# Performance work log

Measured on AMD Instinct MI355X. Metric: run time of the kernel, lower is better.

## Reference

```python
import jax, jax.numpy as jnp
import numpy as np
import math

SIZE = 64
SCALE = math.sqrt(SIZE)
EPS = 1e-12  # torch F.normalize default eps

def l2_normalize(x, axis):
    n = jnp.linalg.norm(x, ord=2, axis=axis, keepdims=True)
    return x / jnp.maximum(n, EPS)

def setup_inputs() -> dict:
    key = jax.random.key(0)
    k1, k2, k3 = jax.random.split(key, 3)
    n, l, s, d, v = 8, 2048, 2048, SIZE, SIZE
    return {
        "query": jax.random.normal(k1, (n, l, d), dtype=jnp.float32),
        "key": jax.random.normal(k2, (n, s, d), dtype=jnp.float32),
        "value": jax.random.normal(k3, (n, s, v), dtype=jnp.float32),
        "mask": jnp.ones((n, l, s), dtype=bool),
    }

def reference(query, key, value, mask):
    # rank-3 query path with normalize=True (cosine attention)
    q = l2_normalize(query, 2)
    k = l2_normalize(key, 2)
    score = jnp.einsum('nlk,nsk->nls', q, k) / SCALE
    score = jnp.where(mask, score, -jnp.inf)
    score = jax.nn.softmax(score, axis=2)  # [n, l, s]
    # equivalent to (score.unsqueeze(3) * value.unsqueeze(1)).sum(2)
    output_value = jnp.einsum('nls,nsv->nlv', score, value)
    return (output_value, score)
```

## Files before the change

kernel.cpp:

```cpp
#include <hip/hip_runtime.h>
#include <hip/hip_bf16.h>
#include <math.h>


typedef __bf16 bf16x8 __attribute__((ext_vector_type(8)));
typedef __bf16 bf16x4 __attribute__((ext_vector_type(4)));
typedef float f32x4 __attribute__((ext_vector_type(4)));

#define NB 8
#define LL 2048
#define SS 2048
#define DD 64
#define MWORDS 64

__global__ __launch_bounds__(512) void prep_mask(const int* __restrict__ mask,
                                                 unsigned* __restrict__ Mb) {
  __shared__ unsigned char nib[512];
  const size_t row = blockIdx.x;
  const int t = threadIdx.x;
  const int4 m = *(const int4*)(mask + row * SS + (size_t)t * 4);
  nib[t] = (unsigned char)((m.x ? 1 : 0) | (m.y ? 2 : 0) | (m.z ? 4 : 0) | (m.w ? 8 : 0));
  __syncthreads();
  if (t < MWORDS) {
    unsigned wd = 0;
#pragma unroll
    for (int i = 0; i < 8; ++i) wd |= (unsigned)nib[t * 8 + i] << (4 * i);
    Mb[row * MWORDS + t] = wd;
  }
}

__global__ __launch_bounds__(256) void prep_norm(const float* __restrict__ q,
                                                 const float* __restrict__ k,
                                                 __bf16* __restrict__ Qb,
                                                 __bf16* __restrict__ Kb) {
  int w = threadIdx.x >> 6, lane = threadIdx.x & 63;
  int r = blockIdx.x * 4 + w;
  const float* src;
  __bf16* dst;
  float extra;
  if (r < NB * LL) {
    src = q + (size_t)r * DD;
    dst = Qb + (size_t)r * DD;
    extra = 0.125f;
  } else {
    int rk = r - NB * LL;
    src = k + (size_t)rk * DD;
    dst = Kb + (size_t)rk * DD;
    extra = 1.0f;
  }
  float x = src[lane];
  float ss = x * x;
  ss += __shfl_xor(ss, 1);
  ss += __shfl_xor(ss, 2);
  ss += __shfl_xor(ss, 4);
  ss += __shfl_xor(ss, 8);
  ss += __shfl_xor(ss, 16);
  ss += __shfl_xor(ss, 32);
  float nrm = sqrtf(ss);
  float sc = extra / fmaxf(nrm, 1e-12f);
  dst[lane] = (__bf16)(x * sc);
}

__global__ __launch_bounds__(256) void prep_vt(const float* __restrict__ v,
                                               __bf16* __restrict__ Vt) {
  __shared__ __bf16 tile[64][72];
  int n = blockIdx.y;
  int s0 = blockIdx.x * 64;
  int t = threadIdx.x;
#pragma unroll
  for (int it = 0; it < 4; ++it) {
    int idx = t + it * 256;
    int s = idx >> 4, c = idx & 15;
    float4 f = *(const float4*)(v + ((size_t)(n * SS + s0 + s)) * DD + c * 4);
    tile[s][c * 4 + 0] = (__bf16)f.x;
    tile[s][c * 4 + 1] = (__bf16)f.y;
    tile[s][c * 4 + 2] = (__bf16)f.z;
    tile[s][c * 4 + 3] = (__bf16)f.w;
  }
  __syncthreads();
#pragma unroll
  for (int it = 0; it < 4; ++it) {
    int idx = t + it * 256;
    int vv = idx >> 4, c = idx & 15;
    bf16x4 o;
    o[0] = tile[c * 4 + 0][vv];
    o[1] = tile[c * 4 + 1][vv];
    o[2] = tile[c * 4 + 2][vv];
    o[3] = tile[c * 4 + 3][vv];
    *(bf16x4*)(Vt + ((size_t)(n * DD + vv)) * SS + s0 + c * 4) = o;
  }
}

__global__ __launch_bounds__(512, 4) void attn_main(const __bf16* __restrict__ Qb,
                                                    const __bf16* __restrict__ Kb,
                                                    const __bf16* __restrict__ Vt,
                                                    const unsigned* __restrict__ Mb,
                                                    float* __restrict__ out_val,
                                                    float* __restrict__ out_score) {
  __shared__ __bf16 e_lds[2][16][136];
  __shared__ float rs_lds[8][16];
  __shared__ float acc_red[4][16][17];

  const int n = blockIdx.y;
  const int l0 = blockIdx.x * 16;
  const int t = threadIdx.x;
  const int w = t >> 6;
  const int lane = t & 63;
  const int m16 = lane & 15;
  const int quad = lane >> 4;
  const int vg = w & 3;
  const int sh = (w >> 2) * 64;

  const __bf16* qrow = Qb + ((size_t)(n * LL + l0 + m16)) * DD;
  bf16x8 aq0 = *(const bf16x8*)(qrow + quad * 8);
  bf16x8 aq1 = *(const bf16x8*)(qrow + 32 + quad * 8);

  const __bf16* kbase = Kb + (size_t)n * SS * DD;
  const __bf16* vrow = Vt + ((size_t)(n * DD + vg * 16 + m16)) * SS + sh;
  const size_t mrow = ((size_t)(n * LL + l0 + m16)) * SS + w * 16 + quad * 4;
  const int off16 = w * 16 + quad * 4;
  const unsigned* mbits = Mb + ((size_t)(n * LL + l0 + m16)) * MWORDS + (off16 >> 5);
  const int bitoff = off16 & 31;

  f32x4 acc_o = {0.f, 0.f, 0.f, 0.f};
  float rsum = 0.f;
  bf16x4 stash[16];
  unsigned bw0 = mbits[0];
  unsigned bw1 = mbits[4];
  unsigned bw2 = mbits[8];
  unsigned bw3 = mbits[12];

#pragma unroll
  for (int c = 0; c < 16; ++c) {
    const int sc = c * 128;
    const int scol = sc + w * 16 + m16;
    const __bf16* krow = kbase + (size_t)scol * DD;
    bf16x8 kb0 = *(const bf16x8*)(krow + quad * 8);
    bf16x8 kb1 = *(const bf16x8*)(krow + 32 + quad * 8);
    bf16x8 bv0 = *(const bf16x8*)(vrow + sc + quad * 8);
    bf16x8 bv1 = *(const bf16x8*)(vrow + sc + 32 + quad * 8);
    f32x4 acc = {0.f, 0.f, 0.f, 0.f};
    acc = __builtin_amdgcn_mfma_f32_16x16x32_bf16(kb0, aq0, acc, 0, 0, 0);
    acc = __builtin_amdgcn_mfma_f32_16x16x32_bf16(kb1, aq1, acc, 0, 0, 0);
    unsigned bits;
    switch (c & 3) {
      case 0: bits = bw0; if (c + 4 < 16) bw0 = mbits[(c + 4) * 4]; break;
      case 1: bits = bw1; if (c + 4 < 16) bw1 = mbits[(c + 4) * 4]; break;
      case 2: bits = bw2; if (c + 4 < 16) bw2 = mbits[(c + 4) * 4]; break;
      default: bits = bw3; if (c + 4 < 16) bw3 = mbits[(c + 4) * 4]; break;
    }
    const unsigned b4 = (bits >> bitoff) & 0xFu;
    float e0 = (b4 & 1u) ? __expf(acc[0]) : 0.f;
    float e1 = (b4 & 2u) ? __expf(acc[1]) : 0.f;
    float e2 = (b4 & 4u) ? __expf(acc[2]) : 0.f;
    float e3 = (b4 & 8u) ? __expf(acc[3]) : 0.f;
    rsum += (e0 + e1) + (e2 + e3);
    bf16x4 sv;
    sv[0] = (__bf16)e0;
    sv[1] = (__bf16)e1;
    sv[2] = (__bf16)e2;
    sv[3] = (__bf16)e3;
    stash[c] = sv;
    *(bf16x4*)(&e_lds[c & 1][m16][w * 16 + quad * 4]) = sv;
    __syncthreads();
    bf16x8 ae0 = *(const bf16x8*)(&e_lds[c & 1][m16][sh + quad * 8]);
    bf16x8 ae1 = *(const bf16x8*)(&e_lds[c & 1][m16][sh + 32 + quad * 8]);
    acc_o = __builtin_amdgcn_mfma_f32_16x16x32_bf16(ae0, bv0, acc_o, 0, 0, 0);
    acc_o = __builtin_amdgcn_mfma_f32_16x16x32_bf16(ae1, bv1, acc_o, 0, 0, 0);
  }

  rsum += __shfl_xor(rsum, 16);
  rsum += __shfl_xor(rsum, 32);
  if (quad == 0) rs_lds[w][m16] = rsum;
  if (w >= 4) {
#pragma unroll
    for (int r = 0; r < 4; ++r) acc_red[vg][quad * 4 + r][m16] = acc_o[r];
  }
  __syncthreads();

  float tot = 0.f;
#pragma unroll
  for (int ww = 0; ww < 8; ++ww) tot += rs_lds[ww][m16];
  const float inv_s = 1.0f / tot;

  if (w < 4) {
#pragma unroll
    for (int r = 0; r < 4; ++r) {
      const int row = quad * 4 + r;
      float tr = 0.f;
#pragma unroll
      for (int ww = 0; ww < 8; ++ww) tr += rs_lds[ww][row];
      const float o = (acc_o[r] + acc_red[vg][row][m16]) / tr;
      out_val[((size_t)(n * LL + l0 + row)) * DD + vg * 16 + m16] = o;
    }
  }

  float* orow = out_score + mrow;
#pragma unroll
  for (int c = 0; c < 16; ++c) {
    float4 o;
    o.x = (float)stash[c][0] * inv_s;
    o.y = (float)stash[c][1] * inv_s;
    o.z = (float)stash[c][2] * inv_s;
    o.w = (float)stash[c][3] * inv_s;
    *(float4*)(orow + (size_t)c * 128) = o;
  }
}

extern "C" void kernel_launch(void* const* d_in, const int* in_sizes, int n_in,
                              void* d_out, int out_size, void* d_ws, size_t ws_size,
                              hipStream_t stream) {
  const float* q = (const float*)d_in[0];
  const float* k = (const float*)d_in[1];
  const float* v = (const float*)d_in[2];
  const int* mask = (const int*)d_in[3];

  float* out_val = (float*)d_out;
  float* out_score = out_val + (size_t)NB * LL * DD;

  __bf16* Qb = (__bf16*)d_ws;
  __bf16* Kb = Qb + (size_t)NB * LL * DD;
  __bf16* Vt = Kb + (size_t)NB * SS * DD;
  unsigned* Mb = (unsigned*)(Vt + (size_t)NB * DD * SS);

  prep_mask<<<dim3(NB * LL), dim3(512), 0, stream>>>(mask, Mb);
  prep_norm<<<dim3((NB * LL * 2) / 4), dim3(256), 0, stream>>>(q, k, Qb, Kb);
  prep_vt<<<dim3(SS / 64, NB), dim3(256), 0, stream>>>(v, Vt);
  attn_main<<<dim3(LL / 16, NB), dim3(512), 0, stream>>>(Qb, Kb, Vt, Mb, out_val, out_score);
}
```

Baseline: 324.2 us.

## Merge prep kernels into one launch, ballot mask packing, nontemporal output stores

Combines the three preprocessing kernels into a single block-partitioned launch, which removes two kernel launches and their tail gaps. The mask is now packed with wave ballots in a grid-stride loop instead of the nibble-in-LDS scheme. The attention grid is flattened so consecutive blocks cycle over the batch index, and the large score and value outputs use nontemporal stores to reduce cache pollution. The mask pass is purely bandwidth bound, so the gain depends mostly on launch overhead and on how well the streaming stores behave.

```diff
diff --git a/kernel.cpp b/kernel.cpp
--- a/kernel.cpp
+++ b/kernel.cpp
@@ -12,82 +12,85 @@
 #define SS 2048
 #define DD 64
 #define MWORDS 64
-
-__global__ __launch_bounds__(512) void prep_mask(const int* __restrict__ mask,
-                                                 unsigned* __restrict__ Mb) {
-  __shared__ unsigned char nib[512];
-  const size_t row = blockIdx.x;
+#define PM_BLOCKS 2048
+#define NORM_BLOCKS ((NB * LL * 2) / 4)
+#define VT_BLOCKS (NB * (SS / 64))
+
+__global__ __launch_bounds__(256) void prep_all(const float* __restrict__ q,
+                                                const float* __restrict__ k,
+                                                const float* __restrict__ v,
+                                                const int* __restrict__ mask,
+                                                __bf16* __restrict__ Qb,
+                                                __bf16* __restrict__ Kb,
+                                                __bf16* __restrict__ Vt,
+                                                unsigned* __restrict__ Mb) {
+  __shared__ __bf16 tile[64][72];
+  const int bid = blockIdx.x;
   const int t = threadIdx.x;
-  const int4 m = *(const int4*)(mask + row * SS + (size_t)t * 4);
-  nib[t] = (unsigned char)((m.x ? 1 : 0) | (m.y ? 2 : 0) | (m.z ? 4 : 0) | (m.w ? 8 : 0));
-  __syncthreads();
-  if (t < MWORDS) {
-    unsigned wd = 0;
-#pragma unroll
-    for (int i = 0; i < 8; ++i) wd |= (unsigned)nib[t * 8 + i] << (4 * i);
-    Mb[row * MWORDS + t] = wd;
-  }
-}
-
-__global__ __launch_bounds__(256) void prep_norm(const float* __restrict__ q,
-                                                 const float* __restrict__ k,
-                                                 __bf16* __restrict__ Qb,
-                                                 __bf16* __restrict__ Kb) {
-  int w = threadIdx.x >> 6, lane = threadIdx.x & 63;
-  int r = blockIdx.x * 4 + w;
-  const float* src;
-  __bf16* dst;
-  float extra;
-  if (r < NB * LL) {
-    src = q + (size_t)r * DD;
-    dst = Qb + (size_t)r * DD;
-    extra = 0.125f;
+
+  if (bid < PM_BLOCKS) {
+    const int lane = t & 63;
+    const size_t total = (size_t)NB * LL * SS;
+    const size_t stride = (size_t)PM_BLOCKS * 256;
+    for (size_t i = (size_t)bid * 256 + t; i < total; i += stride) {
+      int m = mask[i];
+      unsigned long long b = __ballot(m != 0);
+      if ((lane & 31) == 0) Mb[i >> 5] = (unsigned)(b >> (lane & 32));
+    }
+  } else if (bid < PM_BLOCKS + NORM_BLOCKS) {
+    const int nb = bid - PM_BLOCKS;
+    const int w = t >> 6, lane = t & 63;
+    const int r = nb * 4 + w;
+    const float* src;
+    __bf16* dst;
+    float extra;
+    if (r < NB * LL) {
+      src = q + (size_t)r * DD;
+      dst = Qb + (size_t)r * DD;
+      extra = 0.125f;
+    } else {
+      int rk = r - NB * LL;
+      src = k + (size_t)rk * DD;
+      dst = Kb + (size_t)rk * DD;
+      extra = 1.0f;
+    }
+    float x = src[lane];
+    float ss = x * x;
+    ss += __shfl_xor(ss, 1);
+    ss += __shfl_xor(ss, 2);
+    ss += __shfl_xor(ss, 4);
+    ss += __shfl_xor(ss, 8);
+    ss += __shfl_xor(ss, 16);
+    ss += __shfl_xor(ss, 32);
+    float nrm = sqrtf(ss);
+    float sc = extra / fmaxf(nrm, 1e-12f);
+    dst[lane] = (__bf16)(x * sc);
   } else {
-    int rk = r - NB * LL;
-    src = k + (size_t)rk * DD;
-    dst = Kb + (size_t)rk * DD;
-    extra = 1.0f;
-  }
-  float x = src[lane];
-  float ss = x * x;
-  ss += __shfl_xor(ss, 1);
-  ss += __shfl_xor(ss, 2);
-  ss += __shfl_xor(ss, 4);
-  ss += __shfl_xor(ss, 8);
-  ss += __shfl_xor(ss, 16);
-  ss += __shfl_xor(ss, 32);
-  float nrm = sqrtf(ss);
-  float sc = extra / fmaxf(nrm, 1e-12f);
-  dst[lane] = (__bf16)(x * sc);
-}
-
-__global__ __launch_bounds__(256) void prep_vt(const float* __restrict__ v,
-                                               __bf16* __restrict__ Vt) {
-  __shared__ __bf16 tile[64][72];
-  int n = blockIdx.y;
-  int s0 = blockIdx.x * 64;
-  int t = threadIdx.x;
-#pragma unroll
-  for (int it = 0; it < 4; ++it) {
-    int idx = t + it * 256;
-    int s = idx >> 4, c = idx & 15;
-    float4 f = *(const float4*)(v + ((size_t)(n * SS + s0 + s)) * DD + c * 4);
-    tile[s][c * 4 + 0] = (__bf16)f.x;
-    tile[s][c * 4 + 1] = (__bf16)f.y;
-    tile[s][c * 4 + 2] = (__bf16)f.z;
-    tile[s][c * 4 + 3] = (__bf16)f.w;
-  }
-  __syncthreads();
-#pragma unroll
-  for (int it = 0; it < 4; ++it) {
-    int idx = t + it * 256;
-    int vv = idx >> 4, c = idx & 15;
-    bf16x4 o;
-    o[0] = tile[c * 4 + 0][vv];
-    o[1] = tile[c * 4 + 1][vv];
-    o[2] = tile[c * 4 + 2][vv];
-    o[3] = tile[c * 4 + 3][vv];
-    *(bf16x4*)(Vt + ((size_t)(n * DD + vv)) * SS + s0 + c * 4) = o;
+    const int vb = bid - PM_BLOCKS - NORM_BLOCKS;
+    const int n = vb >> 5;
+    const int s0 = (vb & 31) * 64;
+#pragma unroll
+    for (int it = 0; it < 4; ++it) {
+      int idx = t + it * 256;
+      int s = idx >> 4, c = idx & 15;
+      float4 f = *(const float4*)(v + ((size_t)(n * SS + s0 + s)) * DD + c * 4);
+      tile[s][c * 4 + 0] = (__bf16)f.x;
+      tile[s][c * 4 + 1] = (__bf16)f.y;
+      tile[s][c * 4 + 2] = (__bf16)f.z;
+      tile[s][c * 4 + 3] = (__bf16)f.w;
+    }
+    __syncthreads();
+#pragma unroll
+    for (int it = 0; it < 4; ++it) {
+      int idx = t + it * 256;
+      int vv = idx >> 4, c = idx & 15;
+      bf16x4 o;
+      o[0] = tile[c * 4 + 0][vv];
+      o[1] = tile[c * 4 + 1][vv];
+      o[2] = tile[c * 4 + 2][vv];
+      o[3] = tile[c * 4 + 3][vv];
+      *(bf16x4*)(Vt + ((size_t)(n * DD + vv)) * SS + s0 + c * 4) = o;
+    }
   }
 }
 
@@ -101,8 +104,10 @@
   __shared__ float rs_lds[8][16];
   __shared__ float acc_red[4][16][17];
 
-  const int n = blockIdx.y;
-  const int l0 = blockIdx.x * 16;
+  const int id = blockIdx.x;
+  const int n = id & 7;
+  const int l0 = (id >> 3) * 16;
+
   const int t = threadIdx.x;
   const int w = t >> 6;
   const int lane = t & 63;
@@ -191,19 +196,20 @@
 #pragma unroll
       for (int ww = 0; ww < 8; ++ww) tr += rs_lds[ww][row];
       const float o = (acc_o[r] + acc_red[vg][row][m16]) / tr;
-      out_val[((size_t)(n * LL + l0 + row)) * DD + vg * 16 + m16] = o;
+      __builtin_nontemporal_store(
+          o, out_val + ((size_t)(n * LL + l0 + row)) * DD + vg * 16 + m16);
     }
   }
 
   float* orow = out_score + mrow;
 #pragma unroll
   for (int c = 0; c < 16; ++c) {
-    float4 o;
-    o.x = (float)stash[c][0] * inv_s;
-    o.y = (float)stash[c][1] * inv_s;
-    o.z = (float)stash[c][2] * inv_s;
-    o.w = (float)stash[c][3] * inv_s;
-    *(float4*)(orow + (size_t)c * 128) = o;
+    f32x4 o;
+    o[0] = (float)stash[c][0] * inv_s;
+    o[1] = (float)stash[c][1] * inv_s;
+    o[2] = (float)stash[c][2] * inv_s;
+    o[3] = (float)stash[c][3] * inv_s;
+    __builtin_nontemporal_store(o, (f32x4*)(orow + (size_t)c * 128));
   }
 }
 
@@ -223,8 +229,7 @@
   __bf16* Vt = Kb + (size_t)NB * SS * DD;
   unsigned* Mb = (unsigned*)(Vt + (size_t)NB * DD * SS);
 
-  prep_mask<<<dim3(NB * LL), dim3(512), 0, stream>>>(mask, Mb);
-  prep_norm<<<dim3((NB * LL * 2) / 4), dim3(256), 0, stream>>>(q, k, Qb, Kb);
-  prep_vt<<<dim3(SS / 64, NB), dim3(256), 0, stream>>>(v, Vt);
-  attn_main<<<dim3(LL / 16, NB), dim3(512), 0, stream>>>(Qb, Kb, Vt, Mb, out_val, out_score);
+  prep_all<<<dim3(PM_BLOCKS + NORM_BLOCKS + VT_BLOCKS), dim3(256), 0, stream>>>(
+      q, k, v, mask, Qb, Kb, Vt, Mb);
+  attn_main<<<dim3((LL / 16) * NB), dim3(512), 0, stream>>>(Qb, Kb, Vt, Mb, out_val, out_score);
 }
```

After: 333.5 us. +2.9%, slower.
